# Kernel tuning notes

Hardware: AMD Instinct MI355X
Metric: run time of the kernel (lower is better)

The kernel has to match this reference:

```python
import jax, jax.numpy as jnp
import numpy as np

HEADS = 16
DIM = 64  # per-head dim
SCALE = DIM ** (-0.5)


def setup_inputs() -> dict:
    key = jax.random.key(0)
    k1, k2, k3 = jax.random.split(key, 3)
    B, T, E = 2, 2048, 1024
    x = jax.random.normal(k1, (B, T, E), dtype=jnp.float32)
    # torch Linear weights are [out_features, in_features]; init std=0.02
    w_qkv = jax.random.normal(k2, (3 * DIM * HEADS, E), dtype=jnp.float32) * 0.02
    w_out = jax.random.normal(k3, (E, DIM * HEADS), dtype=jnp.float32) * 0.02
    return {"x": x, "w_qkv": w_qkv, "w_out": w_out}


def reference(x, w_qkv, w_out):
    B, T, E = x.shape
    qkv = jnp.einsum('bte,fe->btf', x, w_qkv)  # [B, T, 3*DIM*HEADS]
    # einops 'b t (k d h) -> k b h t d': last dim splits as (k, d, h) with h fastest
    qkv = qkv.reshape(B, T, 3, DIM, HEADS).transpose(2, 0, 4, 1, 3)  # [3, B, H, T, D]
    q, k, v = qkv[0], qkv[1], qkv[2]
    dots = jnp.einsum('bhid,bhjd->bhij', q, k) * SCALE  # [B, H, T, T]
    attn = jax.nn.softmax(dots, axis=-1)
    out = jnp.einsum('bhij,bhjd->bhid', attn, v)  # [B, H, T, D]
    # 'b h t d -> b t (h d)'
    out = out.transpose(0, 2, 1, 3).reshape(B, T, HEADS * DIM)
    return jnp.einsum('btf,ef->bte', out, w_out)  # [B, T, E]
```

## Files before the change

### kernel.cpp

```cpp
#include <hip/hip_runtime.h>
#include <hip/hip_bf16.h>
#include <stdint.h>


using u16 = uint16_t;
typedef __bf16 bf16x8 __attribute__((ext_vector_type(8)));
typedef float f32x4 __attribute__((ext_vector_type(4)));
typedef float f32x16 __attribute__((ext_vector_type(16)));
typedef unsigned short ushort8 __attribute__((ext_vector_type(8)));
typedef uint32_t u32x4 __attribute__((ext_vector_type(4)));
typedef unsigned int u32x2v __attribute__((ext_vector_type(2)));

#define DEV __device__ __forceinline__

typedef __attribute__((address_space(1))) void as1_void;
typedef __attribute__((address_space(3))) void as3_void;

DEV void async16(void* lds_uniform, const void* gsrc) {
    __builtin_amdgcn_global_load_lds((as1_void*)(gsrc), (as3_void*)(lds_uniform), 16, 0, 0);
}

DEV uint16_t f2bf(float x) {
    uint32_t u = __builtin_bit_cast(uint32_t, x);
    u += 0x7fffu + ((u >> 16) & 1u);
    return (uint16_t)(u >> 16);
}

DEV uint32_t pack2(float a, float b) {
    return (uint32_t)f2bf(a) | ((uint32_t)f2bf(b) << 16);
}

DEV uint32_t cvtpk(float lo, float hi) {
    uint32_t r;
    asm("v_cvt_pk_bf16_f32 %0, %1, %2" : "=v"(r) : "v"(lo), "v"(hi));
    return r;
}

DEV float exp2r(float x) { return __builtin_amdgcn_exp2f(x); }

__global__ __launch_bounds__(256) void k_cvt3(const float* __restrict__ x,
                                              const float* __restrict__ wq,
                                              const float* __restrict__ wo,
                                              u16* __restrict__ xb,
                                              u16* __restrict__ wqb,
                                              u16* __restrict__ wob) {
    int i = blockIdx.x * 256 + threadIdx.x;
    const float* in;
    u16* out;
    int j;
    if (i < 524288)       { in = x;  out = xb;  j = i; }
    else if (i < 917504)  { in = wq; out = wqb; j = i - 524288; }
    else                  { in = wo; out = wob; j = i - 917504; }
    const float4* p = (const float4*)in;
    float4 a = p[2 * (size_t)j], b = p[2 * (size_t)j + 1];
    ushort8 o;
    o[0] = f2bf(a.x); o[1] = f2bf(a.y); o[2] = f2bf(a.z); o[3] = f2bf(a.w);
    o[4] = f2bf(b.x); o[5] = f2bf(b.y); o[6] = f2bf(b.z); o[7] = f2bf(b.w);
    *(ushort8*)(out + 8 * (size_t)j) = o;
}

__global__ __launch_bounds__(512) void k_gemm_qkv(const u16* __restrict__ A,
                                                  const u16* __restrict__ B,
                                                  u16* __restrict__ Qp,
                                                  u16* __restrict__ Kp,
                                                  u16* __restrict__ Vtp) {
    __shared__ __align__(16) char smem[81920];
    const int tid = threadIdx.x;
    const int lane = tid & 63, wid = tid >> 6;
    const int r = lane & 15, g = lane >> 4;
    const int wm = wid >> 1, wn = wid & 1;
    const int lin = blockIdx.x;
    const int wg = (lin & 7) * 64 + (lin >> 3);
    const int m0 = (wg >> 4) * 128, n0 = (wg & 15) * 192;

    f32x4 acc[2][6] = {};

    const int colswz = (g ^ (r & 7)) << 4;
    int vA[2], vB[6];
#pragma unroll
    for (int m = 0; m < 2; ++m)
        vA[m] = (wm * 32 + m * 16 + r) * 128 + colswz;
#pragma unroll
    for (int j = 0; j < 6; ++j)
        vB[j] = 32768 + (wn * 96 + j * 16 + r) * 128 + colswz;
    const char* lds = (const char*)smem;

    const int lr = tid >> 3;
    const int scol = (((tid & 7) * 16) ^ ((lr & 7) << 4)) >> 1;
    const u16* aS = A + (size_t)(m0 + lr) * 1024 + scol;
    const u16* bS = B + (size_t)(n0 + lr) * 1024 + scol;
    char* ldsT = (char*)smem + tid * 16;

    auto STAGE_ALL = [&](int buf, int t) {
        const u16* a = aS + t * 64;
        const u16* b = bS + t * 64;
        char* dA = ldsT + buf * 16384;
        char* dB = ldsT + 32768 + buf * 24576;
        async16(dA,          a);
        async16(dA + 8192,   a + 65536);
        async16(dB,          b);
        async16(dB + 8192,   b + 65536);
        async16(dB + 16384,  b + 131072);
    };

    STAGE_ALL(0, 0);

    for (int t = 0; t < 16; ++t) {
        const int buf = t & 1;
        if (t < 15) {
            STAGE_ALL(buf ^ 1, t + 1);
            asm volatile("s_waitcnt vmcnt(5)" ::: "memory");
        } else {
            asm volatile("s_waitcnt vmcnt(0)" ::: "memory");
        }
        __builtin_amdgcn_s_barrier();
        asm volatile("" ::: "memory");

        bf16x8 a[2][2];
#pragma unroll
        for (int m = 0; m < 2; ++m) {
            int ad = buf * 16384 + vA[m];
            a[m][0] = *(const bf16x8*)(lds + ad);
            a[m][1] = *(const bf16x8*)(lds + (ad ^ 64));
        }
        __builtin_amdgcn_s_setprio(1);
#pragma unroll
        for (int j = 0; j < 6; ++j) {
            int bd = buf * 24576 + vB[j];
            bf16x8 b0 = *(const bf16x8*)(lds + bd);
            bf16x8 b1 = *(const bf16x8*)(lds + (bd ^ 64));
#pragma unroll
            for (int m = 0; m < 2; ++m) {
                acc[m][j] = __builtin_amdgcn_mfma_f32_16x16x32_bf16(a[m][0], b0, acc[m][j], 0, 0, 0);
                acc[m][j] = __builtin_amdgcn_mfma_f32_16x16x32_bf16(a[m][1], b1, acc[m][j], 0, 0, 0);
            }
        }
        __builtin_amdgcn_s_setprio(0);
        asm volatile("s_waitcnt lgkmcnt(0)" ::: "memory");
        __builtin_amdgcn_s_barrier();
        asm volatile("" ::: "memory");
    }

#pragma unroll
    for (int jp = 0; jp < 3; ++jp) {
        const int f0 = n0 + wn * 96 + jp * 32;
        const int which = f0 >> 10;
        const int d0 = (f0 & 1023) >> 4;
        if (which < 2) {
            u16* P = which ? Kp : Qp;
#pragma unroll
            for (int m = 0; m < 2; ++m) {
#pragma unroll
                for (int reg = 0; reg < 4; ++reg) {
                    int tt = m0 + wm * 32 + m * 16 + g * 4 + reg;
                    int b = tt >> 11, t = tt & 2047;
                    *(uint32_t*)(P + (((size_t)(b * 16 + r) * 2048 + t) * 64 + d0))
                        = pack2(acc[m][2 * jp][reg], acc[m][2 * jp + 1][reg]);
                }
            }
        } else {
#pragma unroll
            for (int m = 0; m < 2; ++m) {
                int tt0 = m0 + wm * 32 + m * 16 + g * 4;
                int b = tt0 >> 11, t0 = tt0 & 2047;
#pragma unroll
                for (int dj = 0; dj < 2; ++dj) {
                    uint2 val;
                    val.x = pack2(acc[m][2 * jp + dj][0], acc[m][2 * jp + dj][1]);
                    val.y = pack2(acc[m][2 * jp + dj][2], acc[m][2 * jp + dj][3]);
                    *(uint2*)(Vtp + (((size_t)(b * 16 + r) * 64 + d0 + dj) * 2048 + t0)) = val;
                }
            }
        }
    }
}

__global__ __launch_bounds__(512) void k_gemm_out(const u16* __restrict__ A,
                                                  const u16* __restrict__ B,
                                                  float* __restrict__ C) {
    __shared__ __align__(16) char smem[65536];
    const int tid = threadIdx.x;
    const int lane = tid & 63, wid = tid >> 6;
    const int r = lane & 15, g = lane >> 4;
    const int wm = wid >> 2, wn = wid & 3;
    const int lin = blockIdx.x;
    const int wg = (lin & 7) * 32 + (lin >> 3);
    const int m0 = (wg >> 3) * 128, n0 = (wg & 7) * 128;

    f32x4 acc[4][2] = {};

    const int colswz = (g ^ (r & 7)) << 4;
    int vA[4], vB[2];
#pragma unroll
    for (int m = 0; m < 4; ++m) {
        int ii = wm * 64 + m * 16 + r;
        vA[m] = (ii >> 6) * 8192 + (ii & 63) * 128 + colswz;
    }
#pragma unroll
    for (int n = 0; n < 2; ++n) {
        int jj = wn * 32 + n * 16 + r;
        vB[n] = 32768 + (jj >> 6) * 8192 + (jj & 63) * 128 + colswz;
    }
    const char* lds = (const char*)smem;

    const int lr = tid >> 3;
    const int scol = (((tid & 7) * 16) ^ ((lr & 7) << 4)) >> 1;
    const u16* aS = A + (size_t)(m0 + lr) * 1024 + scol;
    const u16* bS = B + (size_t)(n0 + lr) * 1024 + scol;
    char* ldsT = (char*)smem + tid * 16;

    auto STAGE_ALL = [&](int buf, int t) {
        const u16* a = aS + t * 64;
        const u16* b = bS + t * 64;
        async16(ldsT + buf * 16384,          a);
        async16(ldsT + buf * 16384 + 8192,   a + 65536);
        async16(ldsT + 32768 + buf * 16384,        b);
        async16(ldsT + 32768 + buf * 16384 + 8192, b + 65536);
    };

    STAGE_ALL(0, 0);

    for (int t = 0; t < 16; ++t) {
        const int buf = t & 1;
        if (t < 15) {
            STAGE_ALL(buf ^ 1, t + 1);
            asm volatile("s_waitcnt vmcnt(4)" ::: "memory");
        } else {
            asm volatile("s_waitcnt vmcnt(0)" ::: "memory");
        }
        __builtin_amdgcn_s_barrier();
        asm volatile("" ::: "memory");

        bf16x8 a[4][2], b[2][2];
#pragma unroll
        for (int m = 0; m < 4; ++m) {
            int ad = buf * 16384 + vA[m];
            a[m][0] = *(const bf16x8*)(lds + ad);
            a[m][1] = *(const bf16x8*)(lds + (ad ^ 64));
        }
#pragma unroll
        for (int n = 0; n < 2; ++n) {
            int bd = buf * 16384 + vB[n];
            b[n][0] = *(const bf16x8*)(lds + bd);
            b[n][1] = *(const bf16x8*)(lds + (bd ^ 64));
        }
        __builtin_amdgcn_s_setprio(1);
#pragma unroll
        for (int m = 0; m < 4; ++m)
#pragma unroll
            for (int n = 0; n < 2; ++n) {
                acc[m][n] = __builtin_amdgcn_mfma_f32_16x16x32_bf16(a[m][0], b[n][0], acc[m][n], 0, 0, 0);
                acc[m][n] = __builtin_amdgcn_mfma_f32_16x16x32_bf16(a[m][1], b[n][1], acc[m][n], 0, 0, 0);
            }
        __builtin_amdgcn_s_setprio(0);
        asm volatile("s_waitcnt lgkmcnt(0)" ::: "memory");
        __builtin_amdgcn_s_barrier();
        asm volatile("" ::: "memory");
    }

#pragma unroll
    for (int m = 0; m < 4; ++m) {
#pragma unroll
        for (int reg = 0; reg < 4; ++reg) {
            size_t crow = (size_t)(m0 + wm * 64 + m * 16 + g * 4 + reg);
#pragma unroll
            for (int n = 0; n < 2; ++n)
                C[crow * 1024 + n0 + wn * 32 + n * 16 + r] = acc[m][n][reg];
        }
    }
}

__global__ __launch_bounds__(512, 1) void k_attn(const u16* __restrict__ Qp,
                                                 const u16* __restrict__ Kp,
                                                 const u16* __restrict__ Vtp,
                                                 u16* __restrict__ O) {
    constexpr int T = 2048;
    constexpr float ALPHA = 0.18033688f;
    __shared__ __align__(16) char smem[65536];

    const int tid = threadIdx.x;
    const int lane = tid & 63, wv = tid >> 6;
    const int l31 = lane & 31, hi = lane >> 5;

    const int lin = blockIdx.x;
    const int work = (lin & 7) * 32 + (lin >> 3);
    const int bh = work >> 3, qchunk = work & 7;
    const int q0 = qchunk * 256 + wv * 32;

    const u16* Qb = Qp + (size_t)bh * T * 64;
    const u16* Kb = Kp + (size_t)bh * T * 64;
    const u16* Vb = Vtp + (size_t)bh * 64 * T;

    const u16* qrow = Qb + (size_t)(q0 + l31) * 64 + hi * 8;
    bf16x8 qf[4];
#pragma unroll
    for (int kb = 0; kb < 4; ++kb) qf[kb] = *(const bf16x8*)(qrow + kb * 16);

    const char* ldsB = (const char*)smem;
    int off[4];
#pragma unroll
    for (int s = 0; s < 4; ++s)
        off[s] = l31 * 128 + ((((2 * s + hi) ^ (l31 & 7))) << 4);

    const int srow = tid >> 3;
    const int scol = (((tid & 7) * 16) ^ ((srow & 7) << 4)) >> 1;
    const u16* kSrc = Kb + srow * 64 + scol;
    const u16* vSrc = Vb + (size_t)srow * T + scol;
    char* ldsT = smem + tid * 16;

    f32x16 st[2], pex[2], oa[2];
    f32x16 z;
#pragma unroll
    for (int e = 0; e < 16; ++e) { z[e] = 0.f; oa[0][e] = 0.f; oa[1][e] = 0.f; }
    bf16x8 pf[4] = {};
    float lrow = 0.f;

    async16(ldsT, kSrc);
    async16(ldsT + 32768, vSrc);

    for (int it4 = 0; it4 < 8; ++it4) {
#pragma unroll
        for (int sub = 0; sub < 4; ++sub) {
            const int it = it4 * 4 + sub;
            const int KB = sub * 8192;
            const int VBprev = 32768 + ((sub + 3) & 3) * 8192;
            const int KBnext = ((sub + 1) & 3) * 8192;
            const int VBnext = 32768 + ((sub + 1) & 3) * 8192;

            if (it != 31) {
                async16(ldsT + KBnext, kSrc + (size_t)(it + 1) * 4096);
                async16(ldsT + VBnext, vSrc + (it + 1) * 64);
                asm volatile("s_waitcnt vmcnt(3)" ::: "memory");
            } else {
                asm volatile("s_waitcnt vmcnt(0)" ::: "memory");
            }
            __builtin_amdgcn_s_barrier();
            asm volatile("" ::: "memory");

            __builtin_amdgcn_s_setprio(1);
            {
                bf16x8 k0 = *(const bf16x8*)(ldsB + off[0] + KB);
                bf16x8 k1 = *(const bf16x8*)(ldsB + off[0] + KB + 4096);
                st[0] = __builtin_amdgcn_mfma_f32_32x32x16_bf16(k0, qf[0], z, 0, 0, 0);
                st[1] = __builtin_amdgcn_mfma_f32_32x32x16_bf16(k1, qf[0], z, 0, 0, 0);
            }
#pragma unroll
            for (int kb = 1; kb < 4; ++kb) {
                bf16x8 k0 = *(const bf16x8*)(ldsB + off[kb] + KB);
                bf16x8 k1 = *(const bf16x8*)(ldsB + off[kb] + KB + 4096);
                st[0] = __builtin_amdgcn_mfma_f32_32x32x16_bf16(k0, qf[kb], st[0], 0, 0, 0);
                st[1] = __builtin_amdgcn_mfma_f32_32x32x16_bf16(k1, qf[kb], st[1], 0, 0, 0);
            }
            if (it4 + sub != 0) {
#pragma unroll
                for (int jk = 0; jk < 4; ++jk) {
                    bf16x8 v0 = *(const bf16x8*)(ldsB + off[jk] + VBprev);
                    bf16x8 v1 = *(const bf16x8*)(ldsB + off[jk] + VBprev + 4096);
                    oa[0] = __builtin_amdgcn_mfma_f32_32x32x16_bf16(v0, pf[jk], oa[0], 0, 0, 0);
                    oa[1] = __builtin_amdgcn_mfma_f32_32x32x16_bf16(v1, pf[jk], oa[1], 0, 0, 0);
                }
            }
            __builtin_amdgcn_s_setprio(0);

#pragma unroll
            for (int tt = 0; tt < 2; ++tt)
#pragma unroll
                for (int e = 0; e < 16; ++e)
                    pex[tt][e] = exp2r(st[tt][e] * ALPHA);

            float ps0 = 0.f, ps1 = 0.f;
#pragma unroll
            for (int e = 0; e < 16; e += 2) { ps0 += pex[0][e]; ps1 += pex[0][e + 1]; }
#pragma unroll
            for (int e = 0; e < 16; e += 2) { ps0 += pex[1][e]; ps1 += pex[1][e + 1]; }
            lrow += ps0 + ps1;

#pragma unroll
            for (int t = 0; t < 2; ++t) {
                uint32_t c0 = cvtpk(pex[t][0], pex[t][1]);
                uint32_t c1 = cvtpk(pex[t][2], pex[t][3]);
                uint32_t c2 = cvtpk(pex[t][4], pex[t][5]);
                uint32_t c3 = cvtpk(pex[t][6], pex[t][7]);
                uint32_t c4 = cvtpk(pex[t][8], pex[t][9]);
                uint32_t c5 = cvtpk(pex[t][10], pex[t][11]);
                uint32_t c6 = cvtpk(pex[t][12], pex[t][13]);
                uint32_t c7 = cvtpk(pex[t][14], pex[t][15]);
                u32x2v s0 = __builtin_amdgcn_permlane32_swap(c0, c2, false, false);
                u32x2v s1 = __builtin_amdgcn_permlane32_swap(c1, c3, false, false);
                u32x2v s2 = __builtin_amdgcn_permlane32_swap(c4, c6, false, false);
                u32x2v s3 = __builtin_amdgcn_permlane32_swap(c5, c7, false, false);
                u32x4 f0; f0.x = s0[0]; f0.y = s1[0]; f0.z = s0[1]; f0.w = s1[1];
                u32x4 f1; f1.x = s2[0]; f1.y = s3[0]; f1.z = s2[1]; f1.w = s3[1];
                pf[2 * t]     = __builtin_bit_cast(bf16x8, f0);
                pf[2 * t + 1] = __builtin_bit_cast(bf16x8, f1);
            }

            asm volatile("" ::: "memory");
        }
    }

#pragma unroll
    for (int jk = 0; jk < 4; ++jk) {
        bf16x8 v0 = *(const bf16x8*)(ldsB + off[jk] + 57344);
        bf16x8 v1 = *(const bf16x8*)(ldsB + off[jk] + 57344 + 4096);
        oa[0] = __builtin_amdgcn_mfma_f32_32x32x16_bf16(v0, pf[jk], oa[0], 0, 0, 0);
        oa[1] = __builtin_amdgcn_mfma_f32_32x32x16_bf16(v1, pf[jk], oa[1], 0, 0, 0);
    }

    lrow += __shfl_xor(lrow, 32);
    float linv = 1.0f / lrow;
    const int b = bh >> 4, h = bh & 15;
    u16* obase = O + ((size_t)b * T + q0 + l31) * 1024 + h * 64 + 4 * hi;
#pragma unroll
    for (int q = 0; q < 8; ++q) {
        int dbase = ((2 * q) & 3) + 8 * (q >> 1);
        *(uint32_t*)(obase + dbase)      = pack2(oa[0][2 * q] * linv, oa[0][2 * q + 1] * linv);
        *(uint32_t*)(obase + 32 + dbase) = pack2(oa[1][2 * q] * linv, oa[1][2 * q + 1] * linv);
    }
}

extern "C" void kernel_launch(void* const* d_in, const int* in_sizes, int n_in,
                              void* d_out, int out_size, void* d_ws, size_t ws_size,
                              hipStream_t stream) {
    const float* x    = (const float*)d_in[0];
    const float* wqkv = (const float*)d_in[1];
    const float* wout = (const float*)d_in[2];
    float* out = (float*)d_out;
    char* ws = (char*)d_ws;

    u16* xb   = (u16*)(ws);
    u16* wqb  = (u16*)(ws + 8388608);
    u16* wob  = (u16*)(ws + 14680064);
    u16* Qp   = (u16*)(ws + 41943040);
    u16* Kp   = (u16*)(ws + 50331648);
    u16* Vtp  = (u16*)(ws + 58720256);
    u16* Ob   = (u16*)(ws + 67108864);

    k_cvt3<<<4096, 256, 0, stream>>>(x, wqkv, wout, xb, wqb, wob);
    k_gemm_qkv<<<dim3(512), 512, 0, stream>>>(xb, wqb, Qp, Kp, Vtp);
    k_attn<<<dim3(256), dim3(512), 0, stream>>>(Qp, Kp, Vtp, Ob);
    k_gemm_out<<<dim3(256), 512, 0, stream>>>(Ob, wob, out);
}
```

Before: 113.8 us.

## Fold softmax scale into Q, compute row sums via MFMA, load A directly to registers

The QKV GEMM now multiplies Q by the log2e-scaled softmax factor at store time, so the attention kernel can call exp2 directly without a per-element multiply. The attention row-sum is computed with an extra MFMA against a ones vector instead of VALU adds and a cross-lane shuffle. The QKV GEMM warp layout changes to 2x4, and A fragments are loaded from global memory straight into registers instead of being staged in LDS, which cuts LDS use but adds register pressure and uncoalesced global loads. The row sum now comes from bf16-rounded probabilities rather than the fp32 values.

```diff
diff --git a/kernel.cpp b/kernel.cpp
--- a/kernel.cpp
+++ b/kernel.cpp
@@ -64,114 +64,140 @@
                                                   u16* __restrict__ Qp,
                                                   u16* __restrict__ Kp,
                                                   u16* __restrict__ Vtp) {
-    __shared__ __align__(16) char smem[81920];
+    constexpr float QSCALE = 0.18033688f;
+    __shared__ __align__(16) char smem[49152];
     const int tid = threadIdx.x;
     const int lane = tid & 63, wid = tid >> 6;
     const int r = lane & 15, g = lane >> 4;
-    const int wm = wid >> 1, wn = wid & 1;
+    const int wm = wid >> 2, wn = wid & 3;
     const int lin = blockIdx.x;
     const int wg = (lin & 7) * 64 + (lin >> 3);
     const int m0 = (wg >> 4) * 128, n0 = (wg & 15) * 192;
 
-    f32x4 acc[2][6] = {};
+    f32x4 acc[4][3] = {};
 
     const int colswz = (g ^ (r & 7)) << 4;
-    int vA[2], vB[6];
-#pragma unroll
-    for (int m = 0; m < 2; ++m)
-        vA[m] = (wm * 32 + m * 16 + r) * 128 + colswz;
-#pragma unroll
-    for (int j = 0; j < 6; ++j)
-        vB[j] = 32768 + (wn * 96 + j * 16 + r) * 128 + colswz;
+    int vB[3];
+#pragma unroll
+    for (int j = 0; j < 3; ++j)
+        vB[j] = (wn * 48 + j * 16 + r) * 128 + colswz;
+
     const char* lds = (const char*)smem;
+
+    const u16* aP0 = A + (size_t)(m0 + wm * 64 + 0 * 16 + r) * 1024 + g * 8;
+    const u16* aP1 = A + (size_t)(m0 + wm * 64 + 1 * 16 + r) * 1024 + g * 8;
+    const u16* aP2 = A + (size_t)(m0 + wm * 64 + 2 * 16 + r) * 1024 + g * 8;
+    const u16* aP3 = A + (size_t)(m0 + wm * 64 + 3 * 16 + r) * 1024 + g * 8;
 
     const int lr = tid >> 3;
     const int scol = (((tid & 7) * 16) ^ ((lr & 7) << 4)) >> 1;
-    const u16* aS = A + (size_t)(m0 + lr) * 1024 + scol;
     const u16* bS = B + (size_t)(n0 + lr) * 1024 + scol;
     char* ldsT = (char*)smem + tid * 16;
 
-    auto STAGE_ALL = [&](int buf, int t) {
-        const u16* a = aS + t * 64;
+    auto STAGE_B = [&](int buf, int t) {
         const u16* b = bS + t * 64;
-        char* dA = ldsT + buf * 16384;
-        char* dB = ldsT + 32768 + buf * 24576;
-        async16(dA,          a);
-        async16(dA + 8192,   a + 65536);
-        async16(dB,          b);
-        async16(dB + 8192,   b + 65536);
-        async16(dB + 16384,  b + 131072);
-    };
-
-    STAGE_ALL(0, 0);
+        char* d = ldsT + buf * 24576;
+        async16(d,          b);
+        async16(d + 8192,   b + 65536);
+        async16(d + 16384,  b + 131072);
+    };
+
+    bf16x8 aF[4][2];
+    auto LOAD_A = [&](int t) {
+        aF[0][0] = *(const bf16x8*)(aP0 + t * 64);
+        aF[0][1] = *(const bf16x8*)(aP0 + t * 64 + 32);
+        aF[1][0] = *(const bf16x8*)(aP1 + t * 64);
+        aF[1][1] = *(const bf16x8*)(aP1 + t * 64 + 32);
+        aF[2][0] = *(const bf16x8*)(aP2 + t * 64);
+        aF[2][1] = *(const bf16x8*)(aP2 + t * 64 + 32);
+        aF[3][0] = *(const bf16x8*)(aP3 + t * 64);
+        aF[3][1] = *(const bf16x8*)(aP3 + t * 64 + 32);
+    };
+
+    STAGE_B(0, 0);
+    LOAD_A(0);
 
     for (int t = 0; t < 16; ++t) {
         const int buf = t & 1;
         if (t < 15) {
-            STAGE_ALL(buf ^ 1, t + 1);
-            asm volatile("s_waitcnt vmcnt(5)" ::: "memory");
+            STAGE_B(buf ^ 1, t + 1);
+            asm volatile("s_waitcnt vmcnt(3)" ::: "memory");
         } else {
             asm volatile("s_waitcnt vmcnt(0)" ::: "memory");
         }
         __builtin_amdgcn_s_barrier();
         asm volatile("" ::: "memory");
 
-        bf16x8 a[2][2];
-#pragma unroll
-        for (int m = 0; m < 2; ++m) {
-            int ad = buf * 16384 + vA[m];
-            a[m][0] = *(const bf16x8*)(lds + ad);
-            a[m][1] = *(const bf16x8*)(lds + (ad ^ 64));
-        }
         __builtin_amdgcn_s_setprio(1);
 #pragma unroll
-        for (int j = 0; j < 6; ++j) {
+        for (int j = 0; j < 3; ++j) {
             int bd = buf * 24576 + vB[j];
             bf16x8 b0 = *(const bf16x8*)(lds + bd);
             bf16x8 b1 = *(const bf16x8*)(lds + (bd ^ 64));
 #pragma unroll
-            for (int m = 0; m < 2; ++m) {
-                acc[m][j] = __builtin_amdgcn_mfma_f32_16x16x32_bf16(a[m][0], b0, acc[m][j], 0, 0, 0);
-                acc[m][j] = __builtin_amdgcn_mfma_f32_16x16x32_bf16(a[m][1], b1, acc[m][j], 0, 0, 0);
+            for (int m = 0; m < 4; ++m) {
+                acc[m][j] = __builtin_amdgcn_mfma_f32_16x16x32_bf16(aF[m][0], b0, acc[m][j], 0, 0, 0);
+                acc[m][j] = __builtin_amdgcn_mfma_f32_16x16x32_bf16(aF[m][1], b1, acc[m][j], 0, 0, 0);
             }
         }
         __builtin_amdgcn_s_setprio(0);
+        if (t < 15) LOAD_A(t + 1);
         asm volatile("s_waitcnt lgkmcnt(0)" ::: "memory");
         __builtin_amdgcn_s_barrier();
         asm volatile("" ::: "memory");
     }
 
-#pragma unroll
-    for (int jp = 0; jp < 3; ++jp) {
-        const int f0 = n0 + wn * 96 + jp * 32;
-        const int which = f0 >> 10;
-        const int d0 = (f0 & 1023) >> 4;
-        if (which < 2) {
-            u16* P = which ? Kp : Qp;
-#pragma unroll
-            for (int m = 0; m < 2; ++m) {
-#pragma unroll
-                for (int reg = 0; reg < 4; ++reg) {
-                    int tt = m0 + wm * 32 + m * 16 + g * 4 + reg;
-                    int b = tt >> 11, t = tt & 2047;
-                    *(uint32_t*)(P + (((size_t)(b * 16 + r) * 2048 + t) * 64 + d0))
-                        = pack2(acc[m][2 * jp][reg], acc[m][2 * jp + 1][reg]);
-                }
-            }
-        } else {
-#pragma unroll
-            for (int m = 0; m < 2; ++m) {
-                int tt0 = m0 + wm * 32 + m * 16 + g * 4;
-                int b = tt0 >> 11, t0 = tt0 & 2047;
-#pragma unroll
-                for (int dj = 0; dj < 2; ++dj) {
-                    uint2 val;
-                    val.x = pack2(acc[m][2 * jp + dj][0], acc[m][2 * jp + dj][1]);
-                    val.y = pack2(acc[m][2 * jp + dj][2], acc[m][2 * jp + dj][3]);
-                    *(uint2*)(Vtp + (((size_t)(b * 16 + r) * 64 + d0 + dj) * 2048 + t0)) = val;
-                }
-            }
-        }
+    int fv[3], dv[3], wh[3];
+#pragma unroll
+    for (int n = 0; n < 3; ++n) {
+        fv[n] = n0 + wn * 48 + n * 16;
+        wh[n] = fv[n] >> 10;
+        dv[n] = (fv[n] & 1023) >> 4;
+    }
+
+    auto storePairQK = [&](int na) {
+        u16* P = wh[na] ? Kp : Qp;
+        float s = wh[na] ? 1.0f : QSCALE;
+#pragma unroll
+        for (int m = 0; m < 4; ++m)
+#pragma unroll
+            for (int reg = 0; reg < 4; ++reg) {
+                int tt = m0 + wm * 64 + m * 16 + g * 4 + reg;
+                int b = tt >> 11, t = tt & 2047;
+                *(uint32_t*)(P + (((size_t)(b * 16 + r) * 2048 + t) * 64 + dv[na]))
+                    = pack2(acc[m][na][reg] * s, acc[m][na + 1][reg] * s);
+            }
+    };
+    auto storeSoloQK = [&](int n) {
+        u16* P = wh[n] ? Kp : Qp;
+        float s = wh[n] ? 1.0f : QSCALE;
+#pragma unroll
+        for (int m = 0; m < 4; ++m)
+#pragma unroll
+            for (int reg = 0; reg < 4; ++reg) {
+                int tt = m0 + wm * 64 + m * 16 + g * 4 + reg;
+                int b = tt >> 11, t = tt & 2047;
+                P[(((size_t)(b * 16 + r) * 2048 + t) * 64 + dv[n])] = f2bf(acc[m][n][reg] * s);
+            }
+    };
+    auto storeV = [&](int n) {
+#pragma unroll
+        for (int m = 0; m < 4; ++m) {
+            int tt0 = m0 + wm * 64 + m * 16 + g * 4;
+            int b = tt0 >> 11, t0 = tt0 & 2047;
+            uint2 val;
+            val.x = pack2(acc[m][n][0], acc[m][n][1]);
+            val.y = pack2(acc[m][n][2], acc[m][n][3]);
+            *(uint2*)(Vtp + (((size_t)(b * 16 + r) * 64 + dv[n]) * 2048 + t0)) = val;
+        }
+    };
+
+    if ((wn & 1) == 0) {
+        if (wh[0] == 2) { storeV(0); storeV(1); } else storePairQK(0);
+        if (wh[2] == 2) storeV(2); else storeSoloQK(2);
+    } else {
+        if (wh[0] == 2) storeV(0); else storeSoloQK(0);
+        if (wh[1] == 2) { storeV(1); storeV(2); } else storePairQK(1);
     }
 }
 
@@ -275,7 +301,6 @@
                                                  const u16* __restrict__ Vtp,
                                                  u16* __restrict__ O) {
     constexpr int T = 2048;
-    constexpr float ALPHA = 0.18033688f;
     __shared__ __align__(16) char smem[65536];
 
     const int tid = threadIdx.x;
@@ -308,12 +333,15 @@
     const u16* vSrc = Vb + (size_t)srow * T + scol;
     char* ldsT = smem + tid * 16;
 
-    f32x16 st[2], pex[2], oa[2];
+    u32x4 onesu; onesu.x = 0x3F803F80u; onesu.y = 0x3F803F80u;
+    onesu.z = 0x3F803F80u; onesu.w = 0x3F803F80u;
+    const bf16x8 ones8 = __builtin_bit_cast(bf16x8, onesu);
+
+    f32x16 st[2], oa[2], ls;
     f32x16 z;
 #pragma unroll
-    for (int e = 0; e < 16; ++e) { z[e] = 0.f; oa[0][e] = 0.f; oa[1][e] = 0.f; }
+    for (int e = 0; e < 16; ++e) { z[e] = 0.f; oa[0][e] = 0.f; oa[1][e] = 0.f; ls[e] = 0.f; }
     bf16x8 pf[4] = {};
-    float lrow = 0.f;
 
     async16(ldsT, kSrc);
     async16(ldsT + 32768, vSrc);
@@ -358,6 +386,7 @@
                     bf16x8 v1 = *(const bf16x8*)(ldsB + off[jk] + VBprev + 4096);
                     oa[0] = __builtin_amdgcn_mfma_f32_32x32x16_bf16(v0, pf[jk], oa[0], 0, 0, 0);
                     oa[1] = __builtin_amdgcn_mfma_f32_32x32x16_bf16(v1, pf[jk], oa[1], 0, 0, 0);
+                    ls    = __builtin_amdgcn_mfma_f32_32x32x16_bf16(ones8, pf[jk], ls, 0, 0, 0);
                 }
             }
             __builtin_amdgcn_s_setprio(0);
@@ -366,25 +395,18 @@
             for (int tt = 0; tt < 2; ++tt)
 #pragma unroll
                 for (int e = 0; e < 16; ++e)
-                    pex[tt][e] = exp2r(st[tt][e] * ALPHA);
-
-            float ps0 = 0.f, ps1 = 0.f;
-#pragma unroll
-            for (int e = 0; e < 16; e += 2) { ps0 += pex[0][e]; ps1 += pex[0][e + 1]; }
-#pragma unroll
-            for (int e = 0; e < 16; e += 2) { ps0 += pex[1][e]; ps1 += pex[1][e + 1]; }
-            lrow += ps0 + ps1;
+                    st[tt][e] = exp2r(st[tt][e]);
 
 #pragma unroll
             for (int t = 0; t < 2; ++t) {
-                uint32_t c0 = cvtpk(pex[t][0], pex[t][1]);
-                uint32_t c1 = cvtpk(pex[t][2], pex[t][3]);
-                uint32_t c2 = cvtpk(pex[t][4], pex[t][5]);
-                uint32_t c3 = cvtpk(pex[t][6], pex[t][7]);
-                uint32_t c4 = cvtpk(pex[t][8], pex[t][9]);
-                uint32_t c5 = cvtpk(pex[t][10], pex[t][11]);
-                uint32_t c6 = cvtpk(pex[t][12], pex[t][13]);
-                uint32_t c7 = cvtpk(pex[t][14], pex[t][15]);
+                uint32_t c0 = cvtpk(st[t][0], st[t][1]);
+                uint32_t c1 = cvtpk(st[t][2], st[t][3]);
+                uint32_t c2 = cvtpk(st[t][4], st[t][5]);
+                uint32_t c3 = cvtpk(st[t][6], st[t][7]);
+                uint32_t c4 = cvtpk(st[t][8], st[t][9]);
+                uint32_t c5 = cvtpk(st[t][10], st[t][11]);
+                uint32_t c6 = cvtpk(st[t][12], st[t][13]);
+                uint32_t c7 = cvtpk(st[t][14], st[t][15]);
                 u32x2v s0 = __builtin_amdgcn_permlane32_swap(c0, c2, false, false);
                 u32x2v s1 = __builtin_amdgcn_permlane32_swap(c1, c3, false, false);
                 u32x2v s2 = __builtin_amdgcn_permlane32_swap(c4, c6, false, false);
@@ -405,10 +427,10 @@
         bf16x8 v1 = *(const bf16x8*)(ldsB + off[jk] + 57344 + 4096);
         oa[0] = __builtin_amdgcn_mfma_f32_32x32x16_bf16(v0, pf[jk], oa[0], 0, 0, 0);
         oa[1] = __builtin_amdgcn_mfma_f32_32x32x16_bf16(v1, pf[jk], oa[1], 0, 0, 0);
-    }
-
-    lrow += __shfl_xor(lrow, 32);
-    float linv = 1.0f / lrow;
+        ls    = __builtin_amdgcn_mfma_f32_32x32x16_bf16(ones8, pf[jk], ls, 0, 0, 0);
+    }
+
+    float linv = 1.0f / ls[0];
     const int b = bh >> 4, h = bh & 15;
     u16* obase = O + ((size_t)b * T + q0 + l31) * 1024 + h * 64 + 4 * hi;
 #pragma unroll
```

Result: slower. 163.3 us (+43.5%).

## Fold softmax scale into Q, compute row sums via MFMA, deepen K prefetch

Applied to the files above, without the earlier changes.

The softmax scale (times log2e) is folded into Q when the QKV GEMM writes it, which removes a multiply per score in attention. The per-lane VALU row-sum reduction is replaced by an extra MFMA against a ones vector, so the denominator comes from the matrix unit and matches the bf16-rounded probabilities. K tiles are now prefetched two iterations ahead instead of one, and the tail iterations are peeled with explicit waitcnts. The cost is one extra MFMA per PV step, which adds matrix-core load and accumulator registers in a kernel that may already be MFMA-bound.

```diff
diff --git a/kernel.cpp b/kernel.cpp
--- a/kernel.cpp
+++ b/kernel.cpp
@@ -64,6 +64,7 @@
                                                   u16* __restrict__ Qp,
                                                   u16* __restrict__ Kp,
                                                   u16* __restrict__ Vtp) {
+    constexpr float QSCALE = 0.18033688f;
     __shared__ __align__(16) char smem[81920];
     const int tid = threadIdx.x;
     const int lane = tid & 63, wid = tid >> 6;
@@ -146,15 +147,25 @@
         const int f0 = n0 + wn * 96 + jp * 32;
         const int which = f0 >> 10;
         const int d0 = (f0 & 1023) >> 4;
-        if (which < 2) {
-            u16* P = which ? Kp : Qp;
+        if (which == 0) {
 #pragma unroll
             for (int m = 0; m < 2; ++m) {
 #pragma unroll
                 for (int reg = 0; reg < 4; ++reg) {
                     int tt = m0 + wm * 32 + m * 16 + g * 4 + reg;
                     int b = tt >> 11, t = tt & 2047;
-                    *(uint32_t*)(P + (((size_t)(b * 16 + r) * 2048 + t) * 64 + d0))
+                    *(uint32_t*)(Qp + (((size_t)(b * 16 + r) * 2048 + t) * 64 + d0))
+                        = pack2(acc[m][2 * jp][reg] * QSCALE, acc[m][2 * jp + 1][reg] * QSCALE);
+                }
+            }
+        } else if (which == 1) {
+#pragma unroll
+            for (int m = 0; m < 2; ++m) {
+#pragma unroll
+                for (int reg = 0; reg < 4; ++reg) {
+                    int tt = m0 + wm * 32 + m * 16 + g * 4 + reg;
+                    int b = tt >> 11, t = tt & 2047;
+                    *(uint32_t*)(Kp + (((size_t)(b * 16 + r) * 2048 + t) * 64 + d0))
                         = pack2(acc[m][2 * jp][reg], acc[m][2 * jp + 1][reg]);
                 }
             }
@@ -275,7 +286,6 @@
                                                  const u16* __restrict__ Vtp,
                                                  u16* __restrict__ O) {
     constexpr int T = 2048;
-    constexpr float ALPHA = 0.18033688f;
     __shared__ __align__(16) char smem[65536];
 
     const int tid = threadIdx.x;
@@ -308,107 +318,125 @@
     const u16* vSrc = Vb + (size_t)srow * T + scol;
     char* ldsT = smem + tid * 16;
 
-    f32x16 st[2], pex[2], oa[2];
+    u32x4 onesu; onesu.x = 0x3F803F80u; onesu.y = 0x3F803F80u;
+    onesu.z = 0x3F803F80u; onesu.w = 0x3F803F80u;
+    const bf16x8 ones8 = __builtin_bit_cast(bf16x8, onesu);
+
+    f32x16 st[2], oa[2], ls;
     f32x16 z;
 #pragma unroll
-    for (int e = 0; e < 16; ++e) { z[e] = 0.f; oa[0][e] = 0.f; oa[1][e] = 0.f; }
+    for (int e = 0; e < 16; ++e) { z[e] = 0.f; oa[0][e] = 0.f; oa[1][e] = 0.f; ls[e] = 0.f; }
     bf16x8 pf[4] = {};
-    float lrow = 0.f;
+
+    auto body = [&](int KB, int VBprev, bool dopv) {
+        __builtin_amdgcn_s_setprio(1);
+        {
+            bf16x8 k0 = *(const bf16x8*)(ldsB + off[0] + KB);
+            bf16x8 k1 = *(const bf16x8*)(ldsB + off[0] + KB + 4096);
+            st[0] = __builtin_amdgcn_mfma_f32_32x32x16_bf16(k0, qf[0], z, 0, 0, 0);
+            st[1] = __builtin_amdgcn_mfma_f32_32x32x16_bf16(k1, qf[0], z, 0, 0, 0);
+        }
+#pragma unroll
+        for (int kb = 1; kb < 4; ++kb) {
+            bf16x8 k0 = *(const bf16x8*)(ldsB + off[kb] + KB);
+            bf16x8 k1 = *(const bf16x8*)(ldsB + off[kb] + KB + 4096);
+            st[0] = __builtin_amdgcn_mfma_f32_32x32x16_bf16(k0, qf[kb], st[0], 0, 0, 0);
+            st[1] = __builtin_amdgcn_mfma_f32_32x32x16_bf16(k1, qf[kb], st[1], 0, 0, 0);
+        }
+        if (dopv) {
+#pragma unroll
+            for (int jk = 0; jk < 4; ++jk) {
+                bf16x8 v0 = *(const bf16x8*)(ldsB + off[jk] + VBprev);
+                bf16x8 v1 = *(const bf16x8*)(ldsB + off[jk] + VBprev + 4096);
+                oa[0] = __builtin_amdgcn_mfma_f32_32x32x16_bf16(v0, pf[jk], oa[0], 0, 0, 0);
+                oa[1] = __builtin_amdgcn_mfma_f32_32x32x16_bf16(v1, pf[jk], oa[1], 0, 0, 0);
+                ls    = __builtin_amdgcn_mfma_f32_32x32x16_bf16(ones8, pf[jk], ls, 0, 0, 0);
+            }
+        }
+        __builtin_amdgcn_s_setprio(0);
+
+#pragma unroll
+        for (int tt = 0; tt < 2; ++tt)
+#pragma unroll
+            for (int e = 0; e < 16; ++e)
+                st[tt][e] = exp2r(st[tt][e]);
+
+#pragma unroll
+        for (int t2 = 0; t2 < 2; ++t2) {
+            uint32_t c0 = cvtpk(st[t2][0], st[t2][1]);
+            uint32_t c1 = cvtpk(st[t2][2], st[t2][3]);
+            uint32_t c2 = cvtpk(st[t2][4], st[t2][5]);
+            uint32_t c3 = cvtpk(st[t2][6], st[t2][7]);
+            uint32_t c4 = cvtpk(st[t2][8], st[t2][9]);
+            uint32_t c5 = cvtpk(st[t2][10], st[t2][11]);
+            uint32_t c6 = cvtpk(st[t2][12], st[t2][13]);
+            uint32_t c7 = cvtpk(st[t2][14], st[t2][15]);
+            u32x2v s0 = __builtin_amdgcn_permlane32_swap(c0, c2, false, false);
+            u32x2v s1 = __builtin_amdgcn_permlane32_swap(c1, c3, false, false);
+            u32x2v s2 = __builtin_amdgcn_permlane32_swap(c4, c6, false, false);
+            u32x2v s3 = __builtin_amdgcn_permlane32_swap(c5, c7, false, false);
+            u32x4 f0; f0.x = s0[0]; f0.y = s1[0]; f0.z = s0[1]; f0.w = s1[1];
+            u32x4 f1; f1.x = s2[0]; f1.y = s3[0]; f1.z = s2[1]; f1.w = s3[1];
+            pf[2 * t2]     = __builtin_bit_cast(bf16x8, f0);
+            pf[2 * t2 + 1] = __builtin_bit_cast(bf16x8, f1);
+        }
+        asm volatile("" ::: "memory");
+    };
 
     async16(ldsT, kSrc);
     async16(ldsT + 32768, vSrc);
-
-    for (int it4 = 0; it4 < 8; ++it4) {
+    async16(ldsT + 8192, kSrc + 4096);
+
+    for (int it4 = 0; it4 < 7; ++it4) {
 #pragma unroll
         for (int sub = 0; sub < 4; ++sub) {
             const int it = it4 * 4 + sub;
             const int KB = sub * 8192;
             const int VBprev = 32768 + ((sub + 3) & 3) * 8192;
-            const int KBnext = ((sub + 1) & 3) * 8192;
-            const int VBnext = 32768 + ((sub + 1) & 3) * 8192;
-
-            if (it != 31) {
-                async16(ldsT + KBnext, kSrc + (size_t)(it + 1) * 4096);
-                async16(ldsT + VBnext, vSrc + (it + 1) * 64);
-                asm volatile("s_waitcnt vmcnt(3)" ::: "memory");
-            } else {
-                asm volatile("s_waitcnt vmcnt(0)" ::: "memory");
-            }
+            async16(ldsT + ((sub + 2) & 3) * 8192, kSrc + (size_t)(it + 2) * 4096);
+            async16(ldsT + 32768 + ((sub + 1) & 3) * 8192, vSrc + (it + 1) * 64);
+            asm volatile("s_waitcnt vmcnt(4)" ::: "memory");
             __builtin_amdgcn_s_barrier();
             asm volatile("" ::: "memory");
-
-            __builtin_amdgcn_s_setprio(1);
-            {
-                bf16x8 k0 = *(const bf16x8*)(ldsB + off[0] + KB);
-                bf16x8 k1 = *(const bf16x8*)(ldsB + off[0] + KB + 4096);
-                st[0] = __builtin_amdgcn_mfma_f32_32x32x16_bf16(k0, qf[0], z, 0, 0, 0);
-                st[1] = __builtin_amdgcn_mfma_f32_32x32x16_bf16(k1, qf[0], z, 0, 0, 0);
-            }
-#pragma unroll
-            for (int kb = 1; kb < 4; ++kb) {
-                bf16x8 k0 = *(const bf16x8*)(ldsB + off[kb] + KB);
-                bf16x8 k1 = *(const bf16x8*)(ldsB + off[kb] + KB + 4096);
-                st[0] = __builtin_amdgcn_mfma_f32_32x32x16_bf16(k0, qf[kb], st[0], 0, 0, 0);
-                st[1] = __builtin_amdgcn_mfma_f32_32x32x16_bf16(k1, qf[kb], st[1], 0, 0, 0);
-            }
-            if (it4 + sub != 0) {
-#pragma unroll
-                for (int jk = 0; jk < 4; ++jk) {
-                    bf16x8 v0 = *(const bf16x8*)(ldsB + off[jk] + VBprev);
-                    bf16x8 v1 = *(const bf16x8*)(ldsB + off[jk] + VBprev + 4096);
-                    oa[0] = __builtin_amdgcn_mfma_f32_32x32x16_bf16(v0, pf[jk], oa[0], 0, 0, 0);
-                    oa[1] = __builtin_amdgcn_mfma_f32_32x32x16_bf16(v1, pf[jk], oa[1], 0, 0, 0);
-                }
-            }
-            __builtin_amdgcn_s_setprio(0);
-
-#pragma unroll
-            for (int tt = 0; tt < 2; ++tt)
-#pragma unroll
-                for (int e = 0; e < 16; ++e)
-                    pex[tt][e] = exp2r(st[tt][e] * ALPHA);
-
-            float ps0 = 0.f, ps1 = 0.f;
-#pragma unroll
-            for (int e = 0; e < 16; e += 2) { ps0 += pex[0][e]; ps1 += pex[0][e + 1]; }
-#pragma unroll
-            for (int e = 0; e < 16; e += 2) { ps0 += pex[1][e]; ps1 += pex[1][e + 1]; }
-            lrow += ps0 + ps1;
-
-#pragma unroll
-            for (int t = 0; t < 2; ++t) {
-                uint32_t c0 = cvtpk(pex[t][0], pex[t][1]);
-                uint32_t c1 = cvtpk(pex[t][2], pex[t][3]);
-                uint32_t c2 = cvtpk(pex[t][4], pex[t][5]);
-                uint32_t c3 = cvtpk(pex[t][6], pex[t][7]);
-                uint32_t c4 = cvtpk(pex[t][8], pex[t][9]);
-                uint32_t c5 = cvtpk(pex[t][10], pex[t][11]);
-                uint32_t c6 = cvtpk(pex[t][12], pex[t][13]);
-                uint32_t c7 = cvtpk(pex[t][14], pex[t][15]);
-                u32x2v s0 = __builtin_amdgcn_permlane32_swap(c0, c2, false, false);
-                u32x2v s1 = __builtin_amdgcn_permlane32_swap(c1, c3, false, false);
-                u32x2v s2 = __builtin_amdgcn_permlane32_swap(c4, c6, false, false);
-                u32x2v s3 = __builtin_amdgcn_permlane32_swap(c5, c7, false, false);
-                u32x4 f0; f0.x = s0[0]; f0.y = s1[0]; f0.z = s0[1]; f0.w = s1[1];
-                u32x4 f1; f1.x = s2[0]; f1.y = s3[0]; f1.z = s2[1]; f1.w = s3[1];
-                pf[2 * t]     = __builtin_bit_cast(bf16x8, f0);
-                pf[2 * t + 1] = __builtin_bit_cast(bf16x8, f1);
-            }
-
-            asm volatile("" ::: "memory");
-        }
-    }
-
+            body(KB, VBprev, it != 0);
+        }
+    }
+
+    async16(ldsT + 16384, kSrc + (size_t)30 * 4096);
+    async16(ldsT + 32768 + 8192, vSrc + 29 * 64);
+    asm volatile("s_waitcnt vmcnt(4)" ::: "memory");
+    __builtin_amdgcn_s_barrier();
+    asm volatile("" ::: "memory");
+    body(0, 32768 + 24576, true);
+    async16(ldsT + 24576, kSrc + (size_t)31 * 4096);
+    async16(ldsT + 32768 + 16384, vSrc + 30 * 64);
+    asm volatile("s_waitcnt vmcnt(4)" ::: "memory");
+    __builtin_amdgcn_s_barrier();
+    asm volatile("" ::: "memory");
+    body(8192, 32768, true);
+    async16(ldsT + 32768 + 24576, vSrc + 31 * 64);
+    asm volatile("s_waitcnt vmcnt(3)" ::: "memory");
+    __builtin_amdgcn_s_barrier();
+    asm volatile("" ::: "memory");
+    body(16384, 32768 + 8192, true);
+    asm volatile("s_waitcnt vmcnt(1)" ::: "memory");
+    __builtin_amdgcn_s_barrier();
+    asm volatile("" ::: "memory");
+    body(24576, 32768 + 16384, true);
+
+    asm volatile("s_waitcnt vmcnt(0)" ::: "memory");
+    __builtin_amdgcn_s_barrier();
+    asm volatile("" ::: "memory");
 #pragma unroll
     for (int jk = 0; jk < 4; ++jk) {
         bf16x8 v0 = *(const bf16x8*)(ldsB + off[jk] + 57344);
         bf16x8 v1 = *(const bf16x8*)(ldsB + off[jk] + 57344 + 4096);
         oa[0] = __builtin_amdgcn_mfma_f32_32x32x16_bf16(v0, pf[jk], oa[0], 0, 0, 0);
         oa[1] = __builtin_amdgcn_mfma_f32_32x32x16_bf16(v1, pf[jk], oa[1], 0, 0, 0);
-    }
-
-    lrow += __shfl_xor(lrow, 32);
-    float linv = 1.0f / lrow;
+        ls    = __builtin_amdgcn_mfma_f32_32x32x16_bf16(ones8, pf[jk], ls, 0, 0, 0);
+    }
+
+    float linv = 1.0f / ls[0];
     const int b = bh >> 4, h = bh & 15;
     u16* obase = O + ((size_t)b * T + q0 + l31) * 1024 + h * 64 + 4 * hi;
 #pragma unroll
```

Measured after the change: 111.0 us (median of 2 runs). 1.03x faster.
